# Kernel optimization log

Hardware: AMD Instinct MI355X
Metric: run time of the kernel (lower is better)

The kernel has to match this reference:

```python
import jax, jax.numpy as jnp
import numpy as np

N_HEAD = 50000
N_TAIL = 50000
E = 800000
F_IN = 256
D = 64
H = 4
FE = 64
N_ETYPES = 5
NEG_SLOPE = 0.2


def setup_inputs() -> dict:
    key = jax.random.key(0)
    ks = jax.random.split(key, 10)
    head_feature = jax.random.normal(ks[0], (N_HEAD, F_IN), jnp.float32)
    tail_feature = jax.random.normal(ks[1], (N_TAIL, F_IN), jnp.float32)
    head_ind = jax.random.randint(ks[2], (E,), 0, N_HEAD)
    tail_ind = jax.random.randint(ks[3], (E,), 0, N_TAIL)
    edge_list = jnp.stack([head_ind, tail_ind], axis=0)  # [2, E]
    tmp_edge = jax.random.randint(ks[4], (E,), 0, N_ETYPES)
    s = 0.05  # small init scale, mimics uniform(-stdv, stdv)
    W = jax.random.normal(ks[5], (F_IN, D * H), jnp.float32) * s
    W_e = jax.random.normal(ks[6], (FE, FE * H), jnp.float32) * s
    edge_emb = jax.random.normal(ks[7], (N_ETYPES, FE), jnp.float32) * s
    a_l = jax.random.normal(ks[8], (1, H, D), jnp.float32) * s
    a_r = jax.random.normal(jax.random.fold_in(ks[8], 1), (1, H, D), jnp.float32) * s
    a_e = jax.random.normal(ks[9], (1, H, FE), jnp.float32) * s
    return {
        "head_feature": head_feature,
        "tail_feature": tail_feature,
        "edge_list": edge_list,
        "tmp_edge": tmp_edge,
        "W": W,
        "W_e": W_e,
        "edge_emb": edge_emb,
        "a_l": a_l,
        "a_r": a_r,
        "a_e": a_e,
    }


def _layer(head_feature, tail_feature, head_ind, tail_ind, tmp_edge,
           W, W_e, edge_emb, a_l, a_r, a_e):
    n_head = head_feature.shape[0]
    # dense projections (dropout = identity in eval)
    h_head = (head_feature @ W).reshape(-1, H, D)      # [N_h, H, D]
    h_tail = (tail_feature @ W).reshape(-1, H, D)      # [N_t, H, D]
    e = (edge_emb @ W_e).reshape(-1, H, FE)            # [T, H, FE]
    # per-edge attention logits
    h_l = (a_l * h_head).sum(-1)[head_ind]             # [E, H]
    h_r = (a_r * h_tail).sum(-1)[tail_ind]             # [E, H]
    h_e = (a_e * e).sum(-1)[tmp_edge]                  # [E, H]
    score = jax.nn.leaky_relu(h_l + h_r + h_e, NEG_SLOPE)
    # segment softmax over edges grouped by destination (head) node, per head
    m = jax.ops.segment_max(score, head_ind, num_segments=n_head)   # [N_h, H]
    ex = jnp.exp(score - m[head_ind])                               # [E, H]
    z = jax.ops.segment_sum(ex, head_ind, num_segments=n_head)      # [N_h, H]
    alpha = ex / z[head_ind]                                        # [E, H]
    # weighted aggregation: sparse-mm per head, vectorized over heads
    msg = alpha[:, :, None] * h_tail[tail_ind]                      # [E, H, D]
    out = jax.ops.segment_sum(msg, head_ind, num_segments=n_head)   # [N_h, H, D]
    out = out.reshape(n_head, H * D)
    return jax.nn.elu(out)


def reference(head_feature, tail_feature, edge_list, tmp_edge,
              W, W_e, edge_emb, a_l, a_r, a_e):
    head_ind = edge_list[0]
    tail_ind = edge_list[1]
    return _layer(head_feature, tail_feature, head_ind, tail_ind, tmp_edge,
                  W, W_e, edge_emb, a_l, a_r, a_e)
```

## Files before the change

### kernel.cpp

```cpp
#include <hip/hip_runtime.h>
#include <hip/hip_bf16.h>
#include <math.h>

#define N_HEADN 50000
#define N_TAILN 50000
#define NE      800000
#define F_IN    256
#define HH      4
#define HD      256
#define FE      64
#define N_ETYPES 5
#define NEG_SLOPE 0.2f
#define NB_SCAN ((N_HEADN + 255) / 256)
#define NB_CVT  ((N_TAILN * F_IN) / (256 * 16))
#define NB_HIST (NE / 256)
#define NB_PROJ (N_TAILN / 16)

typedef __attribute__((ext_vector_type(8))) short bf16x8;
typedef __attribute__((ext_vector_type(4))) float f32x4;

static __device__ __forceinline__ unsigned short f2bf(float f) {
    unsigned u = __float_as_uint(f);
    return (unsigned short)((u + 0x7FFF + ((u >> 16) & 1)) >> 16);
}
static __device__ __forceinline__ float bf2f(unsigned short u) {
    return __uint_as_float((unsigned)u << 16);
}

__global__ __launch_bounds__(256) void prep_kernel(const int* __restrict__ head,
                                                   int* __restrict__ counts,
                                                   const float* __restrict__ X,
                                                   unsigned short* __restrict__ Xb,
                                                   const float* __restrict__ W,
                                                   const float* __restrict__ a_l,
                                                   const float* __restrict__ W_e,
                                                   const float* __restrict__ a_e,
                                                   const float* __restrict__ edge_emb,
                                                   float* __restrict__ waT,
                                                   float* __restrict__ heo,
                                                   short* __restrict__ Wt) {
    const int b = blockIdx.x;
    if (b < NB_HIST) {
        int e = b * 256 + threadIdx.x;
        atomicAdd(&counts[head[e]], 1);
    } else if (b < NB_HIST + NB_CVT) {
        size_t t = (size_t)(b - NB_HIST) * 256 + threadIdx.x;
        const float4* xp = (const float4*)X + t * 4;
        float4 v0 = xp[0], v1 = xp[1], v2 = xp[2], v3 = xp[3];
        bf16x8 o0, o1;
        o0[0] = (short)f2bf(v0.x); o0[1] = (short)f2bf(v0.y);
        o0[2] = (short)f2bf(v0.z); o0[3] = (short)f2bf(v0.w);
        o0[4] = (short)f2bf(v1.x); o0[5] = (short)f2bf(v1.y);
        o0[6] = (short)f2bf(v1.z); o0[7] = (short)f2bf(v1.w);
        o1[0] = (short)f2bf(v2.x); o1[1] = (short)f2bf(v2.y);
        o1[2] = (short)f2bf(v2.z); o1[3] = (short)f2bf(v2.w);
        o1[4] = (short)f2bf(v3.x); o1[5] = (short)f2bf(v3.y);
        o1[6] = (short)f2bf(v3.z); o1[7] = (short)f2bf(v3.w);
        bf16x8* op = (bf16x8*)(Xb + t * 16);
        op[0] = o0;
        op[1] = o1;
    } else if (b == NB_HIST + NB_CVT) {
        int k = threadIdx.x;
        #pragma unroll
        for (int h = 0; h < HH; ++h) {
            float s = 0.f;
            for (int d = 0; d < 64; ++d) s += a_l[h * 64 + d] * W[(size_t)k * HD + h * 64 + d];
            waT[h * 256 + k] = s;
        }
    } else if (b == NB_HIST + NB_CVT + 1) {
        __shared__ float wae[FE][HH];
        int t = threadIdx.x;
        int k = t >> 2, h = t & 3;
        float s = 0.f;
        for (int f = 0; f < 64; ++f) s += a_e[h * 64 + f] * W_e[(size_t)k * (FE * HH) + h * 64 + f];
        wae[k][h] = s;
        __syncthreads();
        if (t < N_ETYPES * HH) {
            int ty = t >> 2, hh = t & 3;
            float acc = 0.f;
            for (int kk = 0; kk < FE; ++kk) acc += edge_emb[ty * FE + kk] * wae[kk][hh];
            heo[ty * HH + hh] = acc;
        }
    } else {
        int n = b - (NB_HIST + NB_CVT + 2), k = threadIdx.x;
        Wt[(size_t)n * 256 + k] = (short)f2bf(W[(size_t)k * 256 + n]);
    }
}

__global__ void blocksum_kernel(const int* __restrict__ counts, int* __restrict__ blockSums) {
    __shared__ int s[256];
    int t = threadIdx.x, j = blockIdx.x * 256 + t;
    s[t] = (j < N_HEADN) ? counts[j] : 0;
    __syncthreads();
    for (int off = 128; off > 0; off >>= 1) {
        if (t < off) s[t] += s[t + off];
        __syncthreads();
    }
    if (t == 0) blockSums[blockIdx.x] = s[0];
}

__global__ void rowstart_kernel(const int* __restrict__ counts,
                                const int* __restrict__ blockSums,
                                int* __restrict__ row_start, int* __restrict__ cursor) {
    __shared__ int bs[256];
    __shared__ int s[256];
    int t = threadIdx.x, j = blockIdx.x * 256 + t;
    bs[t] = (t < NB_SCAN) ? blockSums[t] : 0;
    __syncthreads();
    for (int off = 1; off < 256; off <<= 1) {
        int u = (t >= off) ? bs[t - off] : 0;
        __syncthreads();
        bs[t] += u;
        __syncthreads();
    }
    const int blockOffV = (blockIdx.x == 0) ? 0 : bs[blockIdx.x - 1];
    int c = (j < N_HEADN) ? counts[j] : 0;
    s[t] = c;
    __syncthreads();
    for (int off = 1; off < 256; off <<= 1) {
        int u = (t >= off) ? s[t - off] : 0;
        __syncthreads();
        s[t] += u;
        __syncthreads();
    }
    int excl = blockOffV + s[t] - c;
    if (j < N_HEADN) {
        row_start[j] = excl;
        cursor[j]    = excl;
        if (j == N_HEADN - 1) row_start[N_HEADN] = excl + c;
    }
}

__global__ __launch_bounds__(256) void head_dot_kernel(const float* __restrict__ X,
                                                       const float* __restrict__ waT,
                                                       float* __restrict__ hl) {
    const int wave = threadIdx.x >> 6;
    const int lane = threadIdx.x & 63;
    const int n = blockIdx.x * 4 + wave;
    float4 x = ((const float4*)(X + (size_t)n * F_IN))[lane];
    float p[HH];
    #pragma unroll
    for (int h = 0; h < HH; ++h) {
        float4 w = ((const float4*)(waT + h * 256))[lane];
        p[h] = x.x * w.x + x.y * w.y + x.z * w.z + x.w * w.w;
    }
    #pragma unroll
    for (int off = 1; off < 64; off <<= 1) {
        #pragma unroll
        for (int h = 0; h < HH; ++h) p[h] += __shfl_xor(p[h], off);
    }
    if (lane < HH) hl[(size_t)n * HH + lane] = p[lane];
}

__global__ __launch_bounds__(256) void proj_mfma_kernel(const unsigned short* __restrict__ Xb,
                                                        const short* __restrict__ Wt,
                                                        const float* __restrict__ a,
                                                        unsigned short* __restrict__ h_out,
                                                        float* __restrict__ hr) {
    const int h    = threadIdx.x >> 6;
    const int lane = threadIdx.x & 63;
    const int quad = lane >> 4;
    const int l15  = lane & 15;
    const int r0   = blockIdx.x * 16;

    const unsigned short* xbase = Xb + (size_t)(r0 + l15) * F_IN + quad * 8;
    bf16x8 xf[8];
    #pragma unroll
    for (int kk = 0; kk < 8; ++kk) xf[kk] = *(const bf16x8*)(xbase + kk * 32);

    f32x4 acc[4];
    #pragma unroll
    for (int ct = 0; ct < 4; ++ct) acc[ct] = (f32x4){0.f, 0.f, 0.f, 0.f};

    const short* wbase = Wt + (size_t)(h * 64 + l15) * 256 + quad * 8;

    #pragma unroll
    for (int kk = 0; kk < 8; ++kk) {
        #pragma unroll
        for (int ct = 0; ct < 4; ++ct) {
            bf16x8 wf = *(const bf16x8*)(wbase + (size_t)ct * 16 * 256 + kk * 32);
            acc[ct] = __builtin_amdgcn_mfma_f32_16x16x32_bf16(wf, xf[kk], acc[ct], 0, 0, 0);
        }
    }

    const int row = r0 + l15;
    float hp = 0.f;
    #pragma unroll
    for (int ct = 0; ct < 4; ++ct) {
        float4 av = *(const float4*)(a + h * 64 + ct * 16 + quad * 4);
        hp += av.x * acc[ct][0] + av.y * acc[ct][1]
            + av.z * acc[ct][2] + av.w * acc[ct][3];
        ushort4 pk;
        pk.x = f2bf(acc[ct][0]); pk.y = f2bf(acc[ct][1]);
        pk.z = f2bf(acc[ct][2]); pk.w = f2bf(acc[ct][3]);
        *(ushort4*)(h_out + (size_t)row * HD + h * 64 + ct * 16 + quad * 4) = pk;
    }
    hp += __shfl_xor(hp, 16);
    hp += __shfl_xor(hp, 32);
    if (lane < 16) hr[(size_t)row * HH + h] = hp;
}

__global__ void scatter_kernel(const int* __restrict__ head, const int* __restrict__ tail,
                               const int* __restrict__ etype,
                               const float* __restrict__ hl, const float* __restrict__ hr,
                               const float* __restrict__ he,
                               int* __restrict__ cursor, int* __restrict__ packed,
                               float* __restrict__ exE) {
    int e = blockIdx.x * 256 + threadIdx.x;
    int h0 = head[e];
    int tl = tail[e];
    int ty = etype[e];
    float4 L = *(const float4*)(hl + (size_t)h0 * HH);
    float4 R = *(const float4*)(hr + (size_t)tl * HH);
    float4 T = *(const float4*)(he + ty * HH);
    float s0 = L.x + R.x + T.x;
    float s1 = L.y + R.y + T.y;
    float s2 = L.z + R.z + T.z;
    float s3 = L.w + R.w + T.w;
    s0 = (s0 > 0.f) ? s0 : NEG_SLOPE * s0;
    s1 = (s1 > 0.f) ? s1 : NEG_SLOPE * s1;
    s2 = (s2 > 0.f) ? s2 : NEG_SLOPE * s2;
    s3 = (s3 > 0.f) ? s3 : NEG_SLOPE * s3;
    float w0 = __expf(s0), w1 = __expf(s1), w2 = __expf(s2), w3 = __expf(s3);
    int pos = atomicAdd(&cursor[h0], 1);
    packed[pos] = tl;
    *(float4*)(exE + (size_t)pos * HH) = make_float4(w0, w1, w2, w3);
}

__global__ __launch_bounds__(256) void agg_kernel(const int* __restrict__ row_start,
                                                  const int* __restrict__ packed,
                                                  const float* __restrict__ exE,
                                                  const unsigned short* __restrict__ h_tail,
                                                  float* __restrict__ out) {
    const int wave = threadIdx.x >> 6;
    const int lane = threadIdx.x & 63;
    const int n = blockIdx.x * 4 + wave;
    const int s = row_start[n];
    const int e = row_start[n + 1];
    const int g = lane >> 5;
    const int q = lane & 31;
    const int h = q >> 3;

    float acc[8];
    #pragma unroll
    for (int c = 0; c < 8; ++c) acc[c] = 0.f;
    float z = 0.f;

    for (int base = s; base < e; base += 64) {
        const int cnt = (e - base < 64) ? (e - base) : 64;
        int myidx = 0;
        if (base + lane < e) myidx = packed[base + lane];
        #pragma unroll 8
        for (int i = 0; i < cnt; i += 2) {
            const int j = i + g;
            const int tl = __shfl(myidx, j);
            if (j < cnt) {
                const float w = exE[(size_t)(base + j) * HH + h];
                uint4 u = *(const uint4*)(h_tail + (size_t)tl * HD + q * 8);
                #pragma unroll
                for (int d = 0; d < 4; ++d) {
                    unsigned uu = ((const unsigned*)&u)[d];
                    acc[2 * d]     += w * __uint_as_float(uu << 16);
                    acc[2 * d + 1] += w * __uint_as_float(uu & 0xFFFF0000u);
                }
                z += w;
            }
        }
    }

    #pragma unroll
    for (int c = 0; c < 8; ++c) acc[c] += __shfl_xor(acc[c], 32);
    z += __shfl_xor(z, 32);

    float4 o;
    if (z > 0.f) {
        o.x = acc[4 * g + 0] / z;
        o.y = acc[4 * g + 1] / z;
        o.z = acc[4 * g + 2] / z;
        o.w = acc[4 * g + 3] / z;
        o.x = (o.x > 0.f) ? o.x : expm1f(o.x);
        o.y = (o.y > 0.f) ? o.y : expm1f(o.y);
        o.z = (o.z > 0.f) ? o.z : expm1f(o.z);
        o.w = (o.w > 0.f) ? o.w : expm1f(o.w);
    } else {
        o = make_float4(0.f, 0.f, 0.f, 0.f);
    }
    ((float4*)(out + (size_t)n * HD))[q * 2 + g] = o;
}

extern "C" void kernel_launch(void* const* d_in, const int* in_sizes, int n_in,
                              void* d_out, int out_size, void* d_ws, size_t ws_size,
                              hipStream_t stream) {
    const float* head_feature = (const float*)d_in[0];
    const float* tail_feature = (const float*)d_in[1];
    const int*   edge_list    = (const int*)d_in[2];
    const int*   tmp_edge     = (const int*)d_in[3];
    const float* W            = (const float*)d_in[4];
    const float* W_e          = (const float*)d_in[5];
    const float* edge_emb     = (const float*)d_in[6];
    const float* a_l          = (const float*)d_in[7];
    const float* a_r          = (const float*)d_in[8];
    const float* a_e          = (const float*)d_in[9];
    const int* head_ind = edge_list;
    const int* tail_ind = edge_list + NE;

    char* ws = (char*)d_ws;
    unsigned short* h_tail = (unsigned short*)ws; ws += sizeof(unsigned short) * (size_t)N_TAILN * HD;
    unsigned short* Xb = (unsigned short*)ws;
    float* exE    = (float*)(void*)Xb;
    int*   packed = (int*)(void*)((char*)(void*)Xb + sizeof(float) * (size_t)NE * HH);
    ws += sizeof(unsigned short) * (size_t)N_TAILN * HD;
    short* Wt        = (short*)ws; ws += sizeof(short) * 256 * 256;
    float* hl        = (float*)ws; ws += sizeof(float) * (size_t)N_HEADN * HH;
    float* hr        = (float*)ws; ws += sizeof(float) * (size_t)N_TAILN * HH;
    float* waT       = (float*)ws; ws += sizeof(float) * HH * 256;
    float* he        = (float*)ws; ws += sizeof(float) * 32;
    int*   counts    = (int*)ws;   ws += sizeof(int) * (size_t)N_HEADN;
    int*   row_start = (int*)ws;   ws += sizeof(int) * (size_t)(N_HEADN + 4);
    int*   cursor    = (int*)ws;   ws += sizeof(int) * (size_t)N_HEADN;
    int*   blockSums = (int*)ws;   ws += sizeof(int) * 256;

    hipMemsetAsync(counts, 0, sizeof(int) * (size_t)N_HEADN, stream);

    hipLaunchKernelGGL(prep_kernel, dim3(NB_HIST + NB_CVT + 258), dim3(256), 0, stream,
                       head_ind, counts, tail_feature, Xb,
                       W, a_l, W_e, a_e, edge_emb, waT, he, Wt);

    hipLaunchKernelGGL(blocksum_kernel, dim3(NB_SCAN), dim3(256), 0, stream,
                       counts, blockSums);
    hipLaunchKernelGGL(rowstart_kernel, dim3(NB_SCAN), dim3(256), 0, stream,
                       counts, blockSums, row_start, cursor);

    hipLaunchKernelGGL(head_dot_kernel, dim3(N_HEADN / 4), dim3(256), 0, stream,
                       head_feature, waT, hl);
    hipLaunchKernelGGL(proj_mfma_kernel, dim3(NB_PROJ), dim3(256), 0, stream,
                       Xb, Wt, a_r, h_tail, hr);

    hipLaunchKernelGGL(scatter_kernel, dim3(NE / 256), dim3(256), 0, stream,
                       head_ind, tail_ind, tmp_edge, hl, hr, he, cursor, packed, exE);

    hipLaunchKernelGGL(agg_kernel, dim3(N_HEADN / 4), dim3(256), 0, stream,
                       row_start, packed, exE, h_tail, (float*)d_out);
}
```

Measured before the change: 379.1 us.

## Stage W in swizzled LDS and run persistent projection blocks with double-buffered X loads

The tail projection kernel now runs as 256 persistent blocks. Each block first copies the full 256x256 bf16 weight matrix (128 KB) into XOR-swizzled shared memory, then loops over row tiles, prefetching the next tile's X fragments while computing the current one. This replaces repeated global/L2 reads of W for every 16-row tile with a single LDS staging per block. The cost is a 128 KB LDS footprint that limits occupancy to one block per CU, plus an upfront copy before any compute starts.

```diff
diff --git a/kernel.cpp b/kernel.cpp
--- a/kernel.cpp
+++ b/kernel.cpp
@@ -14,7 +14,8 @@
 #define NB_SCAN ((N_HEADN + 255) / 256)
 #define NB_CVT  ((N_TAILN * F_IN) / (256 * 16))
 #define NB_HIST (NE / 256)
-#define NB_PROJ (N_TAILN / 16)
+#define NT_PROJ (N_TAILN / 16)
+#define NB_PROJ 256
 
 typedef __attribute__((ext_vector_type(8))) short bf16x8;
 typedef __attribute__((ext_vector_type(4))) float f32x4;
@@ -152,38 +153,47 @@
     if (lane < HH) hl[(size_t)n * HH + lane] = p[lane];
 }
 
-__global__ __launch_bounds__(256) void proj_mfma_kernel(const unsigned short* __restrict__ Xb,
-                                                        const short* __restrict__ Wt,
-                                                        const float* __restrict__ a,
-                                                        unsigned short* __restrict__ h_out,
-                                                        float* __restrict__ hr) {
-    const int h    = threadIdx.x >> 6;
-    const int lane = threadIdx.x & 63;
+struct ProjTileOut { };
+
+static __device__ __forceinline__ void proj_load_xf(const unsigned short* __restrict__ Xb,
+                                                    int tile, int l15, int quad,
+                                                    bf16x8* xf) {
+    const unsigned short* xbase = Xb + (size_t)(tile * 16 + l15) * F_IN + quad * 8;
+    #pragma unroll
+    for (int kk = 0; kk < 8; ++kk) xf[kk] = *(const bf16x8*)(xbase + kk * 32);
+}
+
+static __device__ __forceinline__ void proj_compute(const char* __restrict__ smem,
+                                                    const float* __restrict__ a,
+                                                    unsigned short* __restrict__ h_out,
+                                                    float* __restrict__ hr,
+                                                    int tile, int h, int lane,
+                                                    const bf16x8* xf) {
     const int quad = lane >> 4;
     const int l15  = lane & 15;
-    const int r0   = blockIdx.x * 16;
-
-    const unsigned short* xbase = Xb + (size_t)(r0 + l15) * F_IN + quad * 8;
-    bf16x8 xf[8];
-    #pragma unroll
-    for (int kk = 0; kk < 8; ++kk) xf[kk] = *(const bf16x8*)(xbase + kk * 32);
-
     f32x4 acc[4];
     #pragma unroll
     for (int ct = 0; ct < 4; ++ct) acc[ct] = (f32x4){0.f, 0.f, 0.f, 0.f};
 
-    const short* wbase = Wt + (size_t)(h * 64 + l15) * 256 + quad * 8;
+    int colb[4], sw[4];
+    #pragma unroll
+    for (int ct = 0; ct < 4; ++ct) {
+        int col = h * 64 + ct * 16 + l15;
+        colb[ct] = col * 512;
+        sw[ct]   = col & 31;
+    }
 
     #pragma unroll
     for (int kk = 0; kk < 8; ++kk) {
         #pragma unroll
         for (int ct = 0; ct < 4; ++ct) {
-            bf16x8 wf = *(const bf16x8*)(wbase + (size_t)ct * 16 * 256 + kk * 32);
+            int addr = colb[ct] + ((((quad + kk * 4)) ^ sw[ct]) << 4);
+            bf16x8 wf = *(const bf16x8*)(smem + addr);
             acc[ct] = __builtin_amdgcn_mfma_f32_16x16x32_bf16(wf, xf[kk], acc[ct], 0, 0, 0);
         }
     }
 
-    const int row = r0 + l15;
+    const int row = tile * 16 + l15;
     float hp = 0.f;
     #pragma unroll
     for (int ct = 0; ct < 4; ++ct) {
@@ -198,6 +208,47 @@
     hp += __shfl_xor(hp, 16);
     hp += __shfl_xor(hp, 32);
     if (lane < 16) hr[(size_t)row * HH + h] = hp;
+}
+
+__global__ __launch_bounds__(256) void proj_mfma_kernel(const unsigned short* __restrict__ Xb,
+                                                        const short* __restrict__ Wt,
+                                                        const float* __restrict__ a,
+                                                        unsigned short* __restrict__ h_out,
+                                                        float* __restrict__ hr) {
+    extern __shared__ char smem[];
+    const int h    = threadIdx.x >> 6;
+    const int lane = threadIdx.x & 63;
+    const int l15  = lane & 15;
+    const int quad = lane >> 4;
+
+    int tile = blockIdx.x;
+    bf16x8 xfA[8], xfB[8];
+    if (tile < NT_PROJ) proj_load_xf(Xb, tile, l15, quad, xfA);
+
+    {
+        const int t = threadIdx.x;
+        #pragma unroll
+        for (int i = 0; i < 32; ++i) {
+            int m = i * 256 + t;
+            bf16x8 v = *(const bf16x8*)(Wt + (size_t)m * 8);
+            int col = m >> 5;
+            int c   = m & 31;
+            *(bf16x8*)(smem + col * 512 + ((c ^ (col & 31)) << 4)) = v;
+        }
+    }
+    __syncthreads();
+
+    while (tile < NT_PROJ) {
+        int nxt = tile + NB_PROJ;
+        if (nxt < NT_PROJ) proj_load_xf(Xb, nxt, l15, quad, xfB);
+        proj_compute(smem, a, h_out, hr, tile, h, lane, xfA);
+        tile = nxt;
+        if (tile >= NT_PROJ) break;
+        nxt = tile + NB_PROJ;
+        if (nxt < NT_PROJ) proj_load_xf(Xb, nxt, l15, quad, xfA);
+        proj_compute(smem, a, h_out, hr, tile, h, lane, xfB);
+        tile = nxt;
+    }
 }
 
 __global__ void scatter_kernel(const int* __restrict__ head, const int* __restrict__ tail,
@@ -333,7 +384,14 @@
 
     hipLaunchKernelGGL(head_dot_kernel, dim3(N_HEADN / 4), dim3(256), 0, stream,
                        head_feature, waT, hl);
-    hipLaunchKernelGGL(proj_mfma_kernel, dim3(NB_PROJ), dim3(256), 0, stream,
+
+    static bool lds_attr_set = false;
+    if (!lds_attr_set) {
+        hipFuncSetAttribute((const void*)proj_mfma_kernel,
+                            hipFuncAttributeMaxDynamicSharedMemorySize, 131072);
+        lds_attr_set = true;
+    }
+    hipLaunchKernelGGL(proj_mfma_kernel, dim3(NB_PROJ), dim3(256), 131072, stream,
                        Xb, Wt, a_r, h_tail, hr);
 
     hipLaunchKernelGGL(scatter_kernel, dim3(NE / 256), dim3(256), 0, stream,
```

Result: faster. 332.2 us (-12.4%).
